# Performance work log

Measured on AMD Instinct MI355X. Metric: run time of the kernel, lower is better.

The kernel has to match this reference:

```python
import jax, jax.numpy as jnp
import numpy as np
from itertools import combinations

ADD = 3  # matches init_kwargs

def setup_inputs() -> dict:
    key = jax.random.key(0)
    x = jax.random.uniform(key, (131072, 16), dtype=jnp.float32)
    return {"x": x}

def reference(x) -> jnp.ndarray:
    n = x.shape[1]
    parts = [x]
    for i in range(2, ADD + 1):
        # static index table of all size-i column subsets: [C(n,i), i]
        idx = jnp.asarray(np.array(list(combinations(range(n), i)), dtype=np.int32))
        # gather + reduce: x[:, idx] -> [N, C, i]; Lukasiewicz t-norm = max(sum - (i-1), 0)
        s = jnp.sum(x[:, idx], axis=2)  # [N, C]
        parts.append(jnp.maximum(s - jnp.float32(i - 1), jnp.float32(0)))
    return jnp.concatenate(parts, axis=1)
```

## Files before the change

kernel.cpp:

```cpp
#include <hip/hip_runtime.h>
#include <hip/hip_bf16.h>


#define NCOLS 696
#define NC4   174
#define RPT   16
#define NQUADS (RPT * NC4)

typedef float v4f __attribute__((ext_vector_type(4)));

struct ColTab { unsigned int v[NCOLS]; };

constexpr ColTab make_tab() {
    ColTab t{};
    int k = 0;
    for (int a = 0; a < 16; ++a)
        t.v[k++] = (unsigned)a | (16u << 5) | (16u << 10);
    for (int a = 0; a < 16; ++a)
        for (int b = a + 1; b < 16; ++b)
            t.v[k++] = (unsigned)a | ((unsigned)b << 5) | (16u << 10) | (1u << 15);
    for (int a = 0; a < 16; ++a)
        for (int b = a + 1; b < 16; ++b)
            for (int c = b + 1; c < 16; ++c)
                t.v[k++] = (unsigned)a | ((unsigned)b << 5) | ((unsigned)c << 10) | (2u << 15);
    return t;
}

__constant__ ColTab g_tab = make_tab();

__device__ __forceinline__ float tnorm(const float* __restrict__ xr, unsigned v) {
    return fmaxf(xr[v & 31u] + xr[(v >> 5) & 31u] + xr[(v >> 10) & 31u]
                 - (float)((v >> 15) & 3u), 0.0f);
}

__global__ __launch_bounds__(256) void luk_kernel(const float* __restrict__ x,
                                                  float* __restrict__ out,
                                                  int nrows, int ntiles) {
    __shared__ float xl[RPT * 17];
    const int t = threadIdx.x;
    const uint4* __restrict__ tab4 = reinterpret_cast<const uint4*>(g_tab.v);

    for (int tile = blockIdx.x; tile < ntiles; tile += gridDim.x) {
        const int row0 = tile * RPT;
        const int rlim = min(RPT, nrows - row0);

        {
            const int r = t >> 4, a = t & 15;
            float v = 0.0f;
            if (r < rlim) v = x[(size_t)row0 * 16 + t];
            xl[r * 17 + a] = v;
            if (t < RPT) xl[t * 17 + 16] = 0.0f;
        }
        __syncthreads();

        const int nq = rlim * NC4;
        for (int i = t; i < nq; i += 256) {
            const int r  = (unsigned)i / (unsigned)NC4;
            const int c4 = i - r * NC4;
            const uint4 tv = tab4[c4];
            const float* __restrict__ xr = &xl[r * 17];
            v4f o;
            o.x = tnorm(xr, tv.x);
            o.y = tnorm(xr, tv.y);
            o.z = tnorm(xr, tv.z);
            o.w = tnorm(xr, tv.w);
            v4f* dst = reinterpret_cast<v4f*>(out + (size_t)(row0 + r) * NCOLS) + c4;
            __builtin_nontemporal_store(o, dst);
        }
        __syncthreads();
    }
}

extern "C" void kernel_launch(void* const* d_in, const int* in_sizes, int n_in,
                              void* d_out, int out_size, void* d_ws, size_t ws_size,
                              hipStream_t stream) {
    const float* x = (const float*)d_in[0];
    float* out = (float*)d_out;
    const int nrows  = in_sizes[0] / 16;
    const int ntiles = (nrows + RPT - 1) / RPT;
    const int blocks = ntiles < 2048 ? ntiles : 2048;
    luk_kernel<<<blocks, 256, 0, stream>>>(x, out, nrows, ntiles);
}
```

Measured before the change: 366.7 us.

## Reuse pair sums in LDS to compute triple t-norms with two loads

Computes all pairwise column sums once per row tile, writes the pair outputs, and stores the sums in shared memory. Triple outputs are then formed from one cached pair sum plus one column, using a compact 16-bit index table. This cuts shared-memory loads and arithmetic per output, at the cost of an extra phase and larger LDS usage per block.

```diff
diff --git a/kernel.cpp b/kernel.cpp
--- a/kernel.cpp
+++ b/kernel.cpp
@@ -1,71 +1,105 @@
 #include <hip/hip_runtime.h>
-#include <hip/hip_bf16.h>
 
 
 #define NCOLS 696
-#define NC4   174
 #define RPT   16
-#define NQUADS (RPT * NC4)
+#define RSTR  140
+#define PQ    30
+#define TQ    140
 
 typedef float v4f __attribute__((ext_vector_type(4)));
 
-struct ColTab { unsigned int v[NCOLS]; };
+struct alignas(16) TripTab { unsigned short v[560]; };
+struct alignas(16) PairTab { unsigned short v[120]; };
 
-constexpr ColTab make_tab() {
-    ColTab t{};
-    int k = 0;
-    for (int a = 0; a < 16; ++a)
-        t.v[k++] = (unsigned)a | (16u << 5) | (16u << 10);
+constexpr TripTab make_ttab() {
+    TripTab t{};
+    int pidx[16][16] = {};
+    int pi = 0;
     for (int a = 0; a < 16; ++a)
         for (int b = a + 1; b < 16; ++b)
-            t.v[k++] = (unsigned)a | ((unsigned)b << 5) | (16u << 10) | (1u << 15);
+            pidx[a][b] = pi++;
+    int k = 0;
     for (int a = 0; a < 16; ++a)
         for (int b = a + 1; b < 16; ++b)
             for (int c = b + 1; c < 16; ++c)
-                t.v[k++] = (unsigned)a | ((unsigned)b << 5) | ((unsigned)c << 10) | (2u << 15);
+                t.v[k++] = (unsigned short)((16 + pidx[a][b]) | (c << 8));
+    return t;
+}
+constexpr PairTab make_ptab() {
+    PairTab t{};
+    int k = 0;
+    for (int a = 0; a < 16; ++a)
+        for (int b = a + 1; b < 16; ++b)
+            t.v[k++] = (unsigned short)(a | (b << 5));
     return t;
 }
 
-__constant__ ColTab g_tab = make_tab();
-
-__device__ __forceinline__ float tnorm(const float* __restrict__ xr, unsigned v) {
-    return fmaxf(xr[v & 31u] + xr[(v >> 5) & 31u] + xr[(v >> 10) & 31u]
-                 - (float)((v >> 15) & 3u), 0.0f);
-}
+__constant__ TripTab g_ttab = make_ttab();
+__constant__ PairTab g_ptab = make_ptab();
 
 __global__ __launch_bounds__(256) void luk_kernel(const float* __restrict__ x,
                                                   float* __restrict__ out,
                                                   int nrows, int ntiles) {
-    __shared__ float xl[RPT * 17];
+    __shared__ float L[RPT * RSTR];
     const int t = threadIdx.x;
-    const uint4* __restrict__ tab4 = reinterpret_cast<const uint4*>(g_tab.v);
+    const ushort4* __restrict__ tt4 = reinterpret_cast<const ushort4*>(g_ttab.v);
+    const ushort4* __restrict__ pt4 = reinterpret_cast<const ushort4*>(g_ptab.v);
 
     for (int tile = blockIdx.x; tile < ntiles; tile += gridDim.x) {
         const int row0 = tile * RPT;
         const int rlim = min(RPT, nrows - row0);
+        const size_t obase = (size_t)row0 * NCOLS;
 
         {
             const int r = t >> 4, a = t & 15;
             float v = 0.0f;
             if (r < rlim) v = x[(size_t)row0 * 16 + t];
-            xl[r * 17 + a] = v;
-            if (t < RPT) xl[t * 17 + 16] = 0.0f;
+            L[r * RSTR + a] = v;
         }
         __syncthreads();
 
-        const int nq = rlim * NC4;
+        for (int i = t; i < rlim * PQ; i += 256) {
+            const int r = (unsigned)i / (unsigned)PQ;
+            const int q = i - r * PQ;
+            const ushort4 pv = pt4[q];
+            const float* __restrict__ xr = &L[r * RSTR];
+            const float s0 = xr[pv.x & 31] + xr[pv.x >> 5];
+            const float s1 = xr[pv.y & 31] + xr[pv.y >> 5];
+            const float s2 = xr[pv.z & 31] + xr[pv.z >> 5];
+            const float s3 = xr[pv.w & 31] + xr[pv.w >> 5];
+            v4f sv; sv.x = s0; sv.y = s1; sv.z = s2; sv.w = s3;
+            *reinterpret_cast<v4f*>(&L[r * RSTR + 16 + 4 * q]) = sv;
+            v4f o;
+            o.x = fmaxf(s0 - 1.0f, 0.0f);
+            o.y = fmaxf(s1 - 1.0f, 0.0f);
+            o.z = fmaxf(s2 - 1.0f, 0.0f);
+            o.w = fmaxf(s3 - 1.0f, 0.0f);
+            __builtin_nontemporal_store(
+                o, reinterpret_cast<v4f*>(out + obase + (size_t)r * NCOLS + 16) + q);
+        }
+
+        if (t < rlim * 4) {
+            const int r = t >> 2, q = t & 3;
+            const v4f o = *reinterpret_cast<const v4f*>(&L[r * RSTR + 4 * q]);
+            __builtin_nontemporal_store(
+                o, reinterpret_cast<v4f*>(out + obase + (size_t)r * NCOLS) + q);
+        }
+        __syncthreads();
+
+        const int nq = rlim * TQ;
         for (int i = t; i < nq; i += 256) {
-            const int r  = (unsigned)i / (unsigned)NC4;
-            const int c4 = i - r * NC4;
-            const uint4 tv = tab4[c4];
-            const float* __restrict__ xr = &xl[r * 17];
+            const int r = (unsigned)i / (unsigned)TQ;
+            const int q = i - r * TQ;
+            const ushort4 tv = tt4[q];
+            const float* __restrict__ xr = &L[r * RSTR];
             v4f o;
-            o.x = tnorm(xr, tv.x);
-            o.y = tnorm(xr, tv.y);
-            o.z = tnorm(xr, tv.z);
-            o.w = tnorm(xr, tv.w);
-            v4f* dst = reinterpret_cast<v4f*>(out + (size_t)(row0 + r) * NCOLS) + c4;
-            __builtin_nontemporal_store(o, dst);
+            o.x = fmaxf(xr[tv.x & 255] + xr[tv.x >> 8] - 2.0f, 0.0f);
+            o.y = fmaxf(xr[tv.y & 255] + xr[tv.y >> 8] - 2.0f, 0.0f);
+            o.z = fmaxf(xr[tv.z & 255] + xr[tv.z >> 8] - 2.0f, 0.0f);
+            o.w = fmaxf(xr[tv.w & 255] + xr[tv.w >> 8] - 2.0f, 0.0f);
+            __builtin_nontemporal_store(
+                o, reinterpret_cast<v4f*>(out + obase + (size_t)r * NCOLS + 136) + q);
         }
         __syncthreads();
     }
```

New measurement: 396.2 us. 1.08x slower.
